# Kernel tuning notes

Hardware: AMD Instinct MI355X
Metric: run time of the kernel (lower is better)

The kernel has to match this reference:

```python
import jax, jax.numpy as jnp
import numpy as np

B = 32       # batch
IN_N = 32    # input capsules
IN_D = 16    # input capsule dim (== out_d)
H = 14       # input spatial
OUT_N = 32   # output capsules
OUT_D = 16
HO = 7       # parent grid h_out = w_out
HID = 64     # Linformer projection dim
EPS = 1e-5


def _gconv(x, w, groups):
    # x: [b, C, H, W], w: [C_out, C_in/groups, kh, kw]; stride 1, pad 1
    return jax.lax.conv_general_dilated(
        x, w, window_strides=(1, 1), padding=((1, 1), (1, 1)),
        dimension_numbers=("NCHW", "OIHW", "NCHW"), feature_group_count=groups)


def setup_inputs() -> dict:
    key = jax.random.key(0)
    ks = jax.random.split(key, 7)
    current_pose = jax.random.normal(ks[0], (B, IN_N, H, H, IN_D), dtype=jnp.float32)
    next_pose = jax.random.normal(ks[1], (B, OUT_N, HO, HO, OUT_D), dtype=jnp.float32)
    # grouped conv weights (torch layout OIHW, groups = IN_N)
    current_w = 0.05 * jax.random.normal(ks[2], (IN_N * IN_D, IN_D, 3, 3), dtype=jnp.float32)
    next_w = 0.05 * jax.random.normal(ks[3], (OUT_N * OUT_D, OUT_N * OUT_D // IN_N, 3, 3), dtype=jnp.float32)
    E_proj = 0.02 * jax.random.normal(ks[4], (IN_N, H * H, HID), dtype=jnp.float32)
    rel_embedd = jax.random.normal(ks[5], (IN_D, HO * HO), dtype=jnp.float32)
    ln_gamma = jnp.ones((OUT_D,), dtype=jnp.float32)
    ln_beta = jnp.zeros((OUT_D,), dtype=jnp.float32)
    return {
        "current_pose": current_pose, "next_pose": next_pose,
        "current_w": current_w, "next_w": next_w,
        "E_proj": E_proj, "rel_embedd": rel_embedd,
        "ln_gamma": ln_gamma, "ln_beta": ln_beta,
        "num_iter": 1,
    }


def reference(current_pose, next_pose, current_w, next_w, E_proj, rel_embedd,
              ln_gamma, ln_beta, num_iter):
    b = current_pose.shape[0]
    # 5D -> [b, n*d, H, W]
    cp = current_pose.transpose(0, 2, 3, 1, 4).reshape(b, H, H, IN_N * IN_D)
    cp = cp.transpose(0, 3, 1, 2)
    cp = _gconv(cp, current_w, IN_N)                       # [b, n*d, H, H]
    # headwise Linformer key projection
    cp = cp.reshape(b, IN_D, IN_N, 1, H * H)
    k = jnp.matmul(cp, E_proj)                             # [b, d, n, 1, HID]
    k = k.reshape(b, IN_D, IN_N * HID).transpose(0, 2, 1)  # [b, n*HID, d]
    rel = jnp.broadcast_to(rel_embedd.T[None], (b, HO * HO, IN_D))
    k = jnp.concatenate([k, rel], axis=1)                  # [b, N, d]

    # parent pose -> queries
    q = next_pose.transpose(0, 2, 3, 1, 4).reshape(b, HO, HO, OUT_N * OUT_D)
    q = q.transpose(0, 3, 1, 2)
    q = _gconv(q, next_w, IN_N)                            # [b, out_n*out_d, HO, HO]
    q = q.reshape(b, OUT_N * HO * HO, OUT_D)               # [b, J, d]

    dots = jnp.einsum("bje,bie->bji", q, k) * (IN_D ** -0.5)  # [b, J, N]
    dots = jax.nn.softmax(dots, axis=-2)                   # softmax over queries j
    out = jnp.einsum("bji,bie->bje", dots, k)              # [b, J, d]

    out = out.reshape(b, OUT_N * IN_D, HO, HO)
    out = _gconv(out, next_w, IN_N)
    out = out.reshape(b, OUT_N, HO, HO, IN_D)

    # LayerNorm over last dim (dropout rate = 0)
    mu = out.mean(-1, keepdims=True)
    var = ((out - mu) ** 2).mean(-1, keepdims=True)
    out = (out - mu) / jnp.sqrt(var + EPS) * ln_gamma + ln_beta
    return out
```

## Files before the change

kernel.cpp:

```cpp
#include <hip/hip_runtime.h>

typedef unsigned short u16;
typedef __attribute__((ext_vector_type(8))) short short8;
typedef __attribute__((ext_vector_type(4))) float floatx4;

#define MFMA16(a, b, c) __builtin_amdgcn_mfma_f32_16x16x32_bf16(a, b, c, 0, 0, 0)

__device__ inline u16 bf16rn(float x) {
    unsigned u = __float_as_uint(x);
    u += 0x7fffu + ((u >> 16) & 1u);
    return (u16)(u >> 16);
}
__device__ inline float bf16tof(u16 h) { return __uint_as_float(((unsigned)h) << 16); }
__device__ inline short8 ld8(const u16* p) { return *(const short8*)p; }

__global__ __launch_bounds__(256) void k_conv14(const float* __restrict__ pose,
                                                const float* __restrict__ w,
                                                float* __restrict__ out) {
    int blk = blockIdx.x;
    int tid = threadIdx.x;
    __shared__ float patch[16 * 256];
#pragma unroll
    for (int k = 0; k < 16; ++k) patch[k * 256 + tid] = 0.f;
    __syncthreads();
    const float* pin = pose + (size_t)blk * 3136;
    for (int t = tid; t < 3136; t += 256) {
        int p = t >> 4, ic = t & 15;
        int y = p / 14, x = p % 14;
        patch[ic * 256 + (y + 1) * 16 + (x + 1)] = pin[t];
    }
    __syncthreads();
    int g = blk & 31;
    const float* wg = w + (size_t)g * 2304;
    float* po = out + (size_t)blk * 3136;
    if (tid < 196) {
        int y = tid / 14, x = tid % 14;
        int base = (y + 1) * 16 + (x + 1);
        float acc[16];
#pragma unroll
        for (int oc = 0; oc < 16; ++oc) acc[oc] = 0.f;
        for (int ic = 0; ic < 16; ++ic) {
            const float* pr = patch + ic * 256 + base;
            float win[9];
#pragma unroll
            for (int ky = 0; ky < 3; ++ky)
#pragma unroll
                for (int kx = 0; kx < 3; ++kx)
                    win[ky * 3 + kx] = pr[(ky - 1) * 16 + (kx - 1)];
            const float* wi = wg + ic * 9;
#pragma unroll
            for (int oc = 0; oc < 16; ++oc)
#pragma unroll
                for (int kk = 0; kk < 9; ++kk)
                    acc[oc] += win[kk] * wi[oc * 144 + kk];
        }
#pragma unroll
        for (int oc = 0; oc < 16; ++oc) po[oc * 196 + tid] = acc[oc];
    }
}

__global__ __launch_bounds__(64) void k_conv7(const float* __restrict__ in,
                                              const float* __restrict__ in2,
                                              const float* __restrict__ w,
                                              float* __restrict__ out, int mode) {
    int blk = blockIdx.x;
    int oh = blk & 1, bg = blk >> 1;
    int tid = threadIdx.x;
    __shared__ float patch[16 * 144];
    for (int t = tid; t < 16 * 144; t += 64) patch[t] = 0.f;
    __syncthreads();
    const float* pin = in + (size_t)bg * 784;
    if (mode == 1) {
        for (int t = tid; t < 784; t += 64) {
            int p = t >> 4, ic = t & 15;
            int y = p / 7, x = p % 7;
            patch[ic * 144 + (y + 1) * 16 + (x + 1)] = pin[t];
        }
    } else {
        const float* pin2 = in2 + (size_t)bg * 784;
        for (int t = tid; t < 784; t += 64) {
            int ic = t / 49, p = t % 49;
            int y = p / 7, x = p % 7;
            patch[ic * 144 + (y + 1) * 16 + (x + 1)] = pin[t] + pin2[t];
        }
    }
    __syncthreads();
    int g = bg & 31;
    const float* wg = w + (size_t)g * 2304 + (size_t)oh * 8 * 144;
    float* po = out + (size_t)bg * 784 + (size_t)oh * 8 * 49;
    if (tid < 49) {
        int y = tid / 7, x = tid % 7;
        int base = (y + 1) * 16 + (x + 1);
        float acc[8];
#pragma unroll
        for (int oc = 0; oc < 8; ++oc) acc[oc] = 0.f;
        for (int ic = 0; ic < 16; ++ic) {
            const float* pr = patch + ic * 144 + base;
            float win[9];
#pragma unroll
            for (int ky = 0; ky < 3; ++ky)
#pragma unroll
                for (int kx = 0; kx < 3; ++kx)
                    win[ky * 3 + kx] = pr[(ky - 1) * 16 + (kx - 1)];
            const float* wi = wg + ic * 9;
#pragma unroll
            for (int oc = 0; oc < 8; ++oc)
#pragma unroll
                for (int kk = 0; kk < 9; ++kk)
                    acc[oc] += win[kk] * wi[oc * 144 + kk];
        }
#pragma unroll
        for (int oc = 0; oc < 8; ++oc) po[oc * 49 + tid] = acc[oc];
    }
}

__global__ __launch_bounds__(256) void k_ecvt(const float* __restrict__ E,
                                              u16* __restrict__ EhT,
                                              u16* __restrict__ ElT) {
    __shared__ float ep[196 * 65];
    int m = blockIdx.x, tid = threadIdx.x;
    const float* eb = E + (size_t)m * 12544;
    for (int t = tid; t < 12544; t += 256) {
        int p = t >> 6, h = t & 63;
        ep[p * 65 + h] = eb[t];
    }
    __syncthreads();
    for (int t = tid; t < 64 * 224; t += 256) {
        int h = t / 224, p = t % 224;
        float v = (p < 196) ? ep[p * 65 + h] : 0.f;
        u16 hi = bf16rn(v);
        u16 lo = bf16rn(v - bf16tof(hi));
        EhT[(size_t)m * 14336 + t] = hi;
        ElT[(size_t)m * 14336 + t] = lo;
    }
}

__global__ __launch_bounds__(256) void k_kproj2(const float* __restrict__ cpconv,
                                                const u16* __restrict__ EhT,
                                                const u16* __restrict__ ElT,
                                                u16* __restrict__ Kh,
                                                u16* __restrict__ Kl,
                                                u16* __restrict__ KhT,
                                                u16* __restrict__ KlT) {
    int blk = blockIdx.x;
    int b = blk >> 5, m = blk & 31;
    int wave = threadIdx.x >> 6, lane = threadIdx.x & 63;
    int ht = wave;
    int n = lane & 15, quad = lane >> 4;

    const float* arow = cpconv + ((size_t)b * 512 + (size_t)n * 32 + m) * 196;
    const u16* bhrow = EhT + ((size_t)m * 64 + ht * 16 + n) * 224;
    const u16* blrow = ElT + ((size_t)m * 64 + ht * 16 + n) * 224;

    floatx4 c = {0.f, 0.f, 0.f, 0.f};
#pragma unroll
    for (int pc = 0; pc < 7; ++pc) {
        int p0 = pc * 32 + quad * 8;
        float av[8];
        if (p0 <= 188) {
            float4 x = *(const float4*)(arow + p0);
            float4 y = *(const float4*)(arow + p0 + 4);
            av[0]=x.x; av[1]=x.y; av[2]=x.z; av[3]=x.w;
            av[4]=y.x; av[5]=y.y; av[6]=y.z; av[7]=y.w;
        } else {
#pragma unroll
            for (int k2 = 0; k2 < 8; ++k2) av[k2] = (p0 + k2 < 196) ? arow[p0 + k2] : 0.f;
        }
        short8 ah, al;
#pragma unroll
        for (int k2 = 0; k2 < 8; ++k2) {
            u16 h = bf16rn(av[k2]);
            ah[k2] = (short)h;
            al[k2] = (short)bf16rn(av[k2] - bf16tof(h));
        }
        short8 bh = ld8(bhrow + pc * 32 + quad * 8);
        short8 bl = ld8(blrow + pc * 32 + quad * 8);
        c = MFMA16(ah, bh, c);
        c = MFMA16(ah, bl, c);
        c = MFMA16(al, bh, c);
    }
    int i = m * 64 + ht * 16 + n;
    size_t bK = (size_t)b * 2112;
    size_t bT = (size_t)b * 33792;
    u16 h[4], l[4];
#pragma unroll
    for (int r = 0; r < 4; ++r) {
        h[r] = bf16rn(c[r]);
        l[r] = bf16rn(c[r] - bf16tof(h[r]));
    }
    *(uint2*)(Kh + (bK + i) * 16 + quad * 4) =
        make_uint2((unsigned)h[0] | ((unsigned)h[1] << 16), (unsigned)h[2] | ((unsigned)h[3] << 16));
    *(uint2*)(Kl + (bK + i) * 16 + quad * 4) =
        make_uint2((unsigned)l[0] | ((unsigned)l[1] << 16), (unsigned)l[2] | ((unsigned)l[3] << 16));
#pragma unroll
    for (int r = 0; r < 4; ++r) {
        KhT[bT + (size_t)(quad * 4 + r) * 2112 + i] = h[r];
        KlT[bT + (size_t)(quad * 4 + r) * 2112 + i] = l[r];
    }
}

__global__ __launch_bounds__(256) void k_cvt(const float* __restrict__ qconv,
                                             const float* __restrict__ rel,
                                             u16* __restrict__ Qp,
                                             u16* __restrict__ Kh,
                                             u16* __restrict__ Kl,
                                             u16* __restrict__ KhT,
                                             u16* __restrict__ KlT) {
    int blk = blockIdx.x, tid = threadIdx.x;
    if (blk < 196) {
        int gid = blk * 256 + tid;
        const float4* q4 = (const float4*)(qconv + (size_t)gid * 16);
        float4 t0 = q4[0], t1 = q4[1], t2 = q4[2], t3 = q4[3];
        float v[16] = {t0.x,t0.y,t0.z,t0.w, t1.x,t1.y,t1.z,t1.w,
                       t2.x,t2.y,t2.z,t2.w, t3.x,t3.y,t3.z,t3.w};
        unsigned hw[8], lw[8];
#pragma unroll
        for (int t = 0; t < 8; ++t) {
            float x0 = v[2*t] * 0.25f, x1 = v[2*t+1] * 0.25f;
            u16 h0 = bf16rn(x0), h1 = bf16rn(x1);
            u16 l0 = bf16rn(x0 - bf16tof(h0)), l1 = bf16rn(x1 - bf16tof(h1));
            hw[t] = (unsigned)h0 | ((unsigned)h1 << 16);
            lw[t] = (unsigned)l0 | ((unsigned)l1 << 16);
        }
        uint4* r4 = (uint4*)(Qp + (size_t)gid * 32);
        r4[0] = make_uint4(hw[0], hw[1], hw[2], hw[3]);
        r4[1] = make_uint4(hw[4], hw[5], hw[6], hw[7]);
        r4[2] = make_uint4(lw[0], lw[1], lw[2], lw[3]);
        r4[3] = make_uint4(lw[4], lw[5], lw[6], lw[7]);
    } else {
        int b = blk - 196;
        size_t bK = (size_t)b * 2112;
        size_t bT = (size_t)b * 33792;
#pragma unroll
        for (int k = 0; k < 4; ++k) {
            int idx = tid + k * 256;
            int row = idx >> 4, e = idx & 15;
            int i = 2048 + row;
            float v = (row < 49) ? rel[e * 49 + row] : 0.f;
            u16 h = bf16rn(v);
            u16 l = bf16rn(v - bf16tof(h));
            Kh[(bK + i) * 16 + e] = h;
            Kl[(bK + i) * 16 + e] = l;
            KhT[bT + (size_t)e * 2112 + i] = h;
            KlT[bT + (size_t)e * 2112 + i] = l;
        }
    }
}

__global__ __launch_bounds__(256) void k_stats4(const u16* __restrict__ Qp,
                                                const u16* __restrict__ Kh,
                                                const u16* __restrict__ Kl,
                                                float* __restrict__ dpart) {
    int blk = blockIdx.x;
    int b = blk / 34; int rem = blk % 34; int jh = rem / 17; int tb = rem % 17;
    int wave = threadIdx.x >> 6, lane = threadIdx.x & 63;
    int it2 = tb * 4 + wave;
    if (it2 >= 66) return;
    int ibase = it2 * 32;
    int n = lane & 15, quad = lane >> 4;
    size_t bK = (size_t)b * 2112;
    const u16* kb = Kh + (bK + ibase + n) * 16 + (quad & 1) * 8;
    const u16* lb = Kl + (bK + ibase + n) * 16 + (quad & 1) * 8;
    short8 bh0 = ld8(kb), bh1 = ld8(kb + 256);
    short8 bl0 = ld8(lb), bl1 = ld8(lb + 256);
    const u16* qb = Qp + (size_t)b * 50176 + (size_t)jh * 49 * 512 + n * 32 + quad * 8;
    floatx4 d0 = {0.f,0.f,0.f,0.f}, d1 = {0.f,0.f,0.f,0.f};
    short8 a0 = ld8(qb), a1 = ld8(qb + 512);
    for (int c = 0; c < 49; ++c) {
        short8 a2 = (c + 2 < 49) ? ld8(qb + (size_t)(c + 2) * 512) : a0;
        floatx4 s0 = {0.f,0.f,0.f,0.f}, s1 = {0.f,0.f,0.f,0.f};
        s0 = MFMA16(a0, bh0, s0);
        s0 = MFMA16(a0, bl0, s0);
        s1 = MFMA16(a0, bh1, s1);
        s1 = MFMA16(a0, bl1, s1);
        d0.x += __expf(s0.x); d0.y += __expf(s0.y);
        d0.z += __expf(s0.z); d0.w += __expf(s0.w);
        d1.x += __expf(s1.x); d1.y += __expf(s1.y);
        d1.z += __expf(s1.z); d1.w += __expf(s1.w);
        a0 = a1; a1 = a2;
    }
    float t0 = d0.x + d0.y + d0.z + d0.w;
    float t1 = d1.x + d1.y + d1.z + d1.w;
    t0 += __shfl_xor(t0, 16); t0 += __shfl_xor(t0, 32);
    t1 += __shfl_xor(t1, 16); t1 += __shfl_xor(t1, 32);
    if (quad == 0) {
        dpart[(size_t)jh * 67584 + bK + ibase + n]      = t0;
        dpart[(size_t)jh * 67584 + bK + ibase + 16 + n] = t1;
    }
}

__global__ __launch_bounds__(256) void k_pv4(const u16* __restrict__ Qp,
                                             const u16* __restrict__ Kh,
                                             const u16* __restrict__ Kl,
                                             const u16* __restrict__ KhT,
                                             const u16* __restrict__ KlT,
                                             const float* __restrict__ dpart,
                                             float* __restrict__ opart) {
    __shared__ __align__(16) u16 sH[2][32][2][8];
    __shared__ __align__(16) u16 sL[2][32][2][8];
    __shared__ __align__(16) u16 tH[2][16][32];
    __shared__ __align__(16) u16 tL[2][16][32];
    __shared__ __align__(16) unsigned wbuf[4][16][36];
    __shared__ float rll[2][32];

    int blk = blockIdx.x;
    int b = blk / 50; int rem = blk % 50; int jtb = rem >> 1; int ih = rem & 1;
    int tid = threadIdx.x, wave = tid >> 6, lane = tid & 63;
    int n = lane & 15, quad = lane >> 4, qh = quad & 1;
    int jt = jtb * 4 + wave;
    int jtc = jt < 98 ? jt : 97;
    int i0 = ih * 1056;
    size_t bK = (size_t)b * 2112;
    size_t bT = (size_t)b * 33792;
    const float* d0p = dpart + bK;
    const float* d1p = dpart + 67584 + bK;

    short8 aq = ld8(Qp + ((size_t)b * 1568 + (size_t)jtc * 16 + n) * 32 + quad * 8);

    int role = wave, L = lane;
    uint4 sreg; float dv = 1.f;
    auto ldchunk = [&](int c) {
        int i0c = i0 + c * 32;
        if (role == 0)      sreg = *(const uint4*)(Kh  + (bK + i0c + (L >> 1)) * 16 + (L & 1) * 8);
        else if (role == 1) sreg = *(const uint4*)(Kl  + (bK + i0c + (L >> 1)) * 16 + (L & 1) * 8);
        else if (role == 2) sreg = *(const uint4*)(KhT + bT + (size_t)(L >> 2) * 2112 + i0c + (L & 3) * 8);
        else {
            sreg = *(const uint4*)(KlT + bT + (size_t)(L >> 2) * 2112 + i0c + (L & 3) * 8);
            if (L < 32) dv = d0p[i0c + L] + d1p[i0c + L];
        }
    };
    auto stchunk = [&](int bf) {
        if (role == 0)      *(uint4*)(&sH[bf][L >> 1][L & 1][0]) = sreg;
        else if (role == 1) *(uint4*)(&sL[bf][L >> 1][L & 1][0]) = sreg;
        else if (role == 2) *(uint4*)(&tH[bf][L >> 2][(L & 3) * 8]) = sreg;
        else {
            *(uint4*)(&tL[bf][L >> 2][(L & 3) * 8]) = sreg;
            if (L < 32) rll[bf][L] = 1.0f / dv;
        }
    };

    floatx4 o = {0.f, 0.f, 0.f, 0.f};

    ldchunk(0); stchunk(0); ldchunk(1);
    __syncthreads();
    for (int c = 0; c < 33; ++c) {
        int cb = c & 1;
        short8 sh0 = ld8(&sH[cb][n][qh][0]);
        short8 sh1 = ld8(&sH[cb][16 + n][qh][0]);
        short8 sl0 = ld8(&sL[cb][n][qh][0]);
        short8 sl1 = ld8(&sL[cb][16 + n][qh][0]);
        short8 th  = ld8(&tH[cb][n][quad * 8]);
        short8 tl  = ld8(&tL[cb][n][quad * 8]);
        float r0 = rll[cb][n], r1 = rll[cb][16 + n];
        floatx4 s0 = {0.f,0.f,0.f,0.f};
        s0 = MFMA16(aq, sh0, s0);
        s0 = MFMA16(aq, sl0, s0);
        floatx4 s1 = {0.f,0.f,0.f,0.f};
        s1 = MFMA16(aq, sh1, s1);
        s1 = MFMA16(aq, sl1, s1);
#pragma unroll
        for (int r = 0; r < 4; ++r) {
            float w0 = __expf(s0[r]) * r0;
            float w1 = __expf(s1[r]) * r1;
            unsigned u0 = __float_as_uint(w0), u1 = __float_as_uint(w1);
            unsigned h0 = u0 & 0xffff0000u, h1 = u1 & 0xffff0000u;
            float l0 = w0 - __uint_as_float(h0);
            float l1 = w1 - __uint_as_float(h1);
            wbuf[wave][quad * 4 + r][n]      = h0 | (__float_as_uint(l0) >> 16);
            wbuf[wave][quad * 4 + r][16 + n] = h1 | (__float_as_uint(l1) >> 16);
        }
        asm volatile("s_waitcnt lgkmcnt(0)" ::: "memory");
        uint4 wa = *(const uint4*)(&wbuf[wave][n][quad * 8]);
        uint4 wb = *(const uint4*)(&wbuf[wave][n][quad * 8 + 4]);
        union { unsigned u[4]; short8 s; } hv, lv;
        hv.u[0] = (wa.x >> 16) | (wa.y & 0xffff0000u);
        hv.u[1] = (wa.z >> 16) | (wa.w & 0xffff0000u);
        hv.u[2] = (wb.x >> 16) | (wb.y & 0xffff0000u);
        hv.u[3] = (wb.z >> 16) | (wb.w & 0xffff0000u);
        lv.u[0] = (wa.x & 0xffffu) | (wa.y << 16);
        lv.u[1] = (wa.z & 0xffffu) | (wa.w << 16);
        lv.u[2] = (wb.x & 0xffffu) | (wb.y << 16);
        lv.u[3] = (wb.z & 0xffffu) | (wb.w << 16);
        o = MFMA16(hv.s, th, o);
        o = MFMA16(hv.s, tl, o);
        o = MFMA16(lv.s, th, o);
        if (c < 32) stchunk((c + 1) & 1);
        if (c < 31) ldchunk(c + 2);
        __syncthreads();
    }
    if (jt < 98) {
        float* ob = opart + (size_t)ih * 802816 + ((size_t)b * 1568 + (size_t)jt * 16) * 16;
#pragma unroll
        for (int r = 0; r < 4; ++r) ob[(quad * 4 + r) * 16 + n] = o[r];
    }
}

__global__ __launch_bounds__(256) void k_ln(const float* __restrict__ x,
                                            const float* __restrict__ gamma,
                                            const float* __restrict__ beta,
                                            float* __restrict__ out, int ngroups) {
    int g = blockIdx.x * 256 + threadIdx.x;
    if (g >= ngroups) return;
    const float4* xp = (const float4*)(x + (size_t)g * 16);
    float4 x0 = xp[0], x1 = xp[1], x2 = xp[2], x3 = xp[3];
    float sum = x0.x + x0.y + x0.z + x0.w + x1.x + x1.y + x1.z + x1.w
              + x2.x + x2.y + x2.z + x2.w + x3.x + x3.y + x3.z + x3.w;
    float mu = sum * 0.0625f;
    float var = 0.f;
    var += (x0.x-mu)*(x0.x-mu) + (x0.y-mu)*(x0.y-mu) + (x0.z-mu)*(x0.z-mu) + (x0.w-mu)*(x0.w-mu);
    var += (x1.x-mu)*(x1.x-mu) + (x1.y-mu)*(x1.y-mu) + (x1.z-mu)*(x1.z-mu) + (x1.w-mu)*(x1.w-mu);
    var += (x2.x-mu)*(x2.x-mu) + (x2.y-mu)*(x2.y-mu) + (x2.z-mu)*(x2.z-mu) + (x2.w-mu)*(x2.w-mu);
    var += (x3.x-mu)*(x3.x-mu) + (x3.y-mu)*(x3.y-mu) + (x3.z-mu)*(x3.z-mu) + (x3.w-mu)*(x3.w-mu);
    float rstd = rsqrtf(var * 0.0625f + 1e-5f);
    const float4* gp = (const float4*)gamma;
    const float4* bp = (const float4*)beta;
    float4 g0 = gp[0], g1 = gp[1], g2 = gp[2], g3 = gp[3];
    float4 be0 = bp[0], be1 = bp[1], be2 = bp[2], be3 = bp[3];
    float4 o0, o1, o2, o3;
    o0.x = (x0.x-mu)*rstd*g0.x + be0.x; o0.y = (x0.y-mu)*rstd*g0.y + be0.y;
    o0.z = (x0.z-mu)*rstd*g0.z + be0.z; o0.w = (x0.w-mu)*rstd*g0.w + be0.w;
    o1.x = (x1.x-mu)*rstd*g1.x + be1.x; o1.y = (x1.y-mu)*rstd*g1.y + be1.y;
    o1.z = (x1.z-mu)*rstd*g1.z + be1.z; o1.w = (x1.w-mu)*rstd*g1.w + be1.w;
    o2.x = (x2.x-mu)*rstd*g2.x + be2.x; o2.y = (x2.y-mu)*rstd*g2.y + be2.y;
    o2.z = (x2.z-mu)*rstd*g2.z + be2.z; o2.w = (x2.w-mu)*rstd*g2.w + be2.w;
    o3.x = (x3.x-mu)*rstd*g3.x + be3.x; o3.y = (x3.y-mu)*rstd*g3.y + be3.y;
    o3.z = (x3.z-mu)*rstd*g3.z + be3.z; o3.w = (x3.w-mu)*rstd*g3.w + be3.w;
    float4* op = (float4*)(out + (size_t)g * 16);
    op[0] = o0; op[1] = o1; op[2] = o2; op[3] = o3;
}

extern "C" void kernel_launch(void* const* d_in, const int* in_sizes, int n_in,
                              void* d_out, int out_size, void* d_ws, size_t ws_size,
                              hipStream_t stream) {
    const float* current_pose = (const float*)d_in[0];
    const float* next_pose    = (const float*)d_in[1];
    const float* current_w    = (const float*)d_in[2];
    const float* next_w       = (const float*)d_in[3];
    const float* E_proj       = (const float*)d_in[4];
    const float* rel          = (const float*)d_in[5];
    const float* ln_gamma     = (const float*)d_in[6];
    const float* ln_beta      = (const float*)d_in[7];
    float* out = (float*)d_out;
    float* ws  = (float*)d_ws;

    float* cpconv = ws;
    float* conv2  = ws;
    float* opart  = ws + 802816;
    float* dpart  = ws + 2408448;
    float* qconv  = ws + 3211264;
    u16*   ub     = (u16*)(ws + 4014080);
    u16* Qp  = ub;
    u16* Kh  = ub + 1605632;
    u16* Kl  = ub + 2686976;
    u16* KhT = ub + 3768320;
    u16* KlT = ub + 4849664;
    u16* EhT = ub + 5931008;
    u16* ElT = ub + 6389760;

    k_conv14<<<1024, 256, 0, stream>>>(current_pose, current_w, cpconv);
    k_conv7 <<<2048, 64,  0, stream>>>(next_pose, next_pose, next_w, qconv, 1);
    k_ecvt  <<<32,   256, 0, stream>>>(E_proj, EhT, ElT);
    k_cvt   <<<228,  256, 0, stream>>>(qconv, rel, Qp, Kh, Kl, KhT, KlT);
    k_kproj2<<<1024, 256, 0, stream>>>(cpconv, EhT, ElT, Kh, Kl, KhT, KlT);
    k_stats4<<<1088, 256, 0, stream>>>(Qp, Kh, Kl, dpart);
    k_pv4   <<<1600, 256, 0, stream>>>(Qp, Kh, Kl, KhT, KlT, dpart, opart);
    k_conv7 <<<2048, 64,  0, stream>>>(opart, opart + 802816, next_w, conv2, 0);
    k_ln    <<<196,  256, 0, stream>>>(conv2, ln_gamma, ln_beta, out, 50176);
}
```

Baseline: 245.0 us.

## Merge preprocessing kernels, split conv14 across output halves, single-bf16 softmax weights

Folds the E_proj conversion, the rel-embedding K rows and a weight re-layout for the 14x14 grouped conv into one preprocessing kernel. conv14 now runs twice as many blocks, each computing 8 output channels with the reordered weights so each block reads a contiguous run of weights. In the PV kernel the softmax weights are truncated to a single bf16 instead of a hi/lo pair, cutting one MFMA and the packing work per chunk. The truncation lowers the accuracy of the attention output, and halving conv14 means each input patch is loaded twice.

```diff
diff --git a/kernel.cpp b/kernel.cpp
--- a/kernel.cpp
+++ b/kernel.cpp
@@ -14,31 +14,88 @@
 __device__ inline float bf16tof(u16 h) { return __uint_as_float(((unsigned)h) << 16); }
 __device__ inline short8 ld8(const u16* p) { return *(const short8*)p; }
 
+__global__ __launch_bounds__(256) void k_ecvt2(const float* __restrict__ E,
+                                               const float* __restrict__ rel,
+                                               const float* __restrict__ w,
+                                               u16* __restrict__ EhT,
+                                               u16* __restrict__ ElT,
+                                               u16* __restrict__ Kh,
+                                               u16* __restrict__ Kl,
+                                               u16* __restrict__ KhT,
+                                               u16* __restrict__ KlT,
+                                               float* __restrict__ w2) {
+    int blk = blockIdx.x, tid = threadIdx.x;
+    if (blk < 32) {
+        __shared__ float ep[196 * 65];
+        int m = blk;
+        const float* eb = E + (size_t)m * 12544;
+        for (int t = tid; t < 12544; t += 256) {
+            int p = t >> 6, h = t & 63;
+            ep[p * 65 + h] = eb[t];
+        }
+        __syncthreads();
+        for (int t = tid; t < 64 * 224; t += 256) {
+            int h = t / 224, p = t % 224;
+            float v = (p < 196) ? ep[p * 65 + h] : 0.f;
+            u16 hi = bf16rn(v);
+            u16 lo = bf16rn(v - bf16tof(hi));
+            EhT[(size_t)m * 14336 + t] = hi;
+            ElT[(size_t)m * 14336 + t] = lo;
+        }
+    } else if (blk < 64) {
+        int b = blk - 32;
+        size_t bK = (size_t)b * 2112;
+        size_t bT = (size_t)b * 33792;
+#pragma unroll
+        for (int k = 0; k < 4; ++k) {
+            int idx = tid + k * 256;
+            int row = idx >> 4, e = idx & 15;
+            int i = 2048 + row;
+            float v = (row < 49) ? rel[e * 49 + row] : 0.f;
+            u16 h = bf16rn(v);
+            u16 l = bf16rn(v - bf16tof(h));
+            Kh[(bK + i) * 16 + e] = h;
+            Kl[(bK + i) * 16 + e] = l;
+            KhT[bT + (size_t)e * 2112 + i] = h;
+            KlT[bT + (size_t)e * 2112 + i] = l;
+        }
+    } else {
+        int g0 = (blk - 64) * 4;
+        for (int t = tid; t < 4 * 2304; t += 256) {
+            int g = g0 + t / 2304, r = t % 2304;
+            int oc = r / 144, rr = r % 144;
+            w2[(size_t)g * 2304 + (rr / 9) * 144 + oc * 9 + (rr % 9)] =
+                w[(size_t)g * 2304 + r];
+        }
+    }
+}
+
 __global__ __launch_bounds__(256) void k_conv14(const float* __restrict__ pose,
-                                                const float* __restrict__ w,
+                                                const float* __restrict__ w2,
                                                 float* __restrict__ out) {
     int blk = blockIdx.x;
+    int oh = blk & 1, bg = blk >> 1;
     int tid = threadIdx.x;
     __shared__ float patch[16 * 256];
 #pragma unroll
     for (int k = 0; k < 16; ++k) patch[k * 256 + tid] = 0.f;
     __syncthreads();
-    const float* pin = pose + (size_t)blk * 3136;
+    const float* pin = pose + (size_t)bg * 3136;
     for (int t = tid; t < 3136; t += 256) {
         int p = t >> 4, ic = t & 15;
         int y = p / 14, x = p % 14;
         patch[ic * 256 + (y + 1) * 16 + (x + 1)] = pin[t];
     }
     __syncthreads();
-    int g = blk & 31;
-    const float* wg = w + (size_t)g * 2304;
-    float* po = out + (size_t)blk * 3136;
+    int g = bg & 31;
+    const float* wg = w2 + (size_t)g * 2304 + oh * 72;
+    float* po = out + (size_t)bg * 3136 + oh * 8 * 196;
     if (tid < 196) {
         int y = tid / 14, x = tid % 14;
         int base = (y + 1) * 16 + (x + 1);
-        float acc[16];
-#pragma unroll
-        for (int oc = 0; oc < 16; ++oc) acc[oc] = 0.f;
+        float acc[8];
+#pragma unroll
+        for (int oc = 0; oc < 8; ++oc) acc[oc] = 0.f;
         for (int ic = 0; ic < 16; ++ic) {
             const float* pr = patch + ic * 256 + base;
             float win[9];
@@ -47,15 +104,15 @@
 #pragma unroll
                 for (int kx = 0; kx < 3; ++kx)
                     win[ky * 3 + kx] = pr[(ky - 1) * 16 + (kx - 1)];
-            const float* wi = wg + ic * 9;
-#pragma unroll
-            for (int oc = 0; oc < 16; ++oc)
+            const float* wi = wg + ic * 144;
+#pragma unroll
+            for (int oc = 0; oc < 8; ++oc)
 #pragma unroll
                 for (int kk = 0; kk < 9; ++kk)
-                    acc[oc] += win[kk] * wi[oc * 144 + kk];
-        }
-#pragma unroll
-        for (int oc = 0; oc < 16; ++oc) po[oc * 196 + tid] = acc[oc];
+                    acc[oc] += win[kk] * wi[oc * 9 + kk];
+        }
+#pragma unroll
+        for (int oc = 0; oc < 8; ++oc) po[oc * 196 + tid] = acc[oc];
     }
 }
 
@@ -114,27 +171,6 @@
     }
 }
 
-__global__ __launch_bounds__(256) void k_ecvt(const float* __restrict__ E,
-                                              u16* __restrict__ EhT,
-                                              u16* __restrict__ ElT) {
-    __shared__ float ep[196 * 65];
-    int m = blockIdx.x, tid = threadIdx.x;
-    const float* eb = E + (size_t)m * 12544;
-    for (int t = tid; t < 12544; t += 256) {
-        int p = t >> 6, h = t & 63;
-        ep[p * 65 + h] = eb[t];
-    }
-    __syncthreads();
-    for (int t = tid; t < 64 * 224; t += 256) {
-        int h = t / 224, p = t % 224;
-        float v = (p < 196) ? ep[p * 65 + h] : 0.f;
-        u16 hi = bf16rn(v);
-        u16 lo = bf16rn(v - bf16tof(hi));
-        EhT[(size_t)m * 14336 + t] = hi;
-        ElT[(size_t)m * 14336 + t] = lo;
-    }
-}
-
 __global__ __launch_bounds__(256) void k_kproj2(const float* __restrict__ cpconv,
                                                 const u16* __restrict__ EhT,
                                                 const u16* __restrict__ ElT,
@@ -200,51 +236,26 @@
 }
 
 __global__ __launch_bounds__(256) void k_cvt(const float* __restrict__ qconv,
-                                             const float* __restrict__ rel,
-                                             u16* __restrict__ Qp,
-                                             u16* __restrict__ Kh,
-                                             u16* __restrict__ Kl,
-                                             u16* __restrict__ KhT,
-                                             u16* __restrict__ KlT) {
-    int blk = blockIdx.x, tid = threadIdx.x;
-    if (blk < 196) {
-        int gid = blk * 256 + tid;
-        const float4* q4 = (const float4*)(qconv + (size_t)gid * 16);
-        float4 t0 = q4[0], t1 = q4[1], t2 = q4[2], t3 = q4[3];
-        float v[16] = {t0.x,t0.y,t0.z,t0.w, t1.x,t1.y,t1.z,t1.w,
-                       t2.x,t2.y,t2.z,t2.w, t3.x,t3.y,t3.z,t3.w};
-        unsigned hw[8], lw[8];
-#pragma unroll
-        for (int t = 0; t < 8; ++t) {
-            float x0 = v[2*t] * 0.25f, x1 = v[2*t+1] * 0.25f;
-            u16 h0 = bf16rn(x0), h1 = bf16rn(x1);
-            u16 l0 = bf16rn(x0 - bf16tof(h0)), l1 = bf16rn(x1 - bf16tof(h1));
-            hw[t] = (unsigned)h0 | ((unsigned)h1 << 16);
-            lw[t] = (unsigned)l0 | ((unsigned)l1 << 16);
-        }
-        uint4* r4 = (uint4*)(Qp + (size_t)gid * 32);
-        r4[0] = make_uint4(hw[0], hw[1], hw[2], hw[3]);
-        r4[1] = make_uint4(hw[4], hw[5], hw[6], hw[7]);
-        r4[2] = make_uint4(lw[0], lw[1], lw[2], lw[3]);
-        r4[3] = make_uint4(lw[4], lw[5], lw[6], lw[7]);
-    } else {
-        int b = blk - 196;
-        size_t bK = (size_t)b * 2112;
-        size_t bT = (size_t)b * 33792;
-#pragma unroll
-        for (int k = 0; k < 4; ++k) {
-            int idx = tid + k * 256;
-            int row = idx >> 4, e = idx & 15;
-            int i = 2048 + row;
-            float v = (row < 49) ? rel[e * 49 + row] : 0.f;
-            u16 h = bf16rn(v);
-            u16 l = bf16rn(v - bf16tof(h));
-            Kh[(bK + i) * 16 + e] = h;
-            Kl[(bK + i) * 16 + e] = l;
-            KhT[bT + (size_t)e * 2112 + i] = h;
-            KlT[bT + (size_t)e * 2112 + i] = l;
-        }
-    }
+                                             u16* __restrict__ Qp) {
+    int gid = blockIdx.x * 256 + threadIdx.x;
+    const float4* q4 = (const float4*)(qconv + (size_t)gid * 16);
+    float4 t0 = q4[0], t1 = q4[1], t2 = q4[2], t3 = q4[3];
+    float v[16] = {t0.x,t0.y,t0.z,t0.w, t1.x,t1.y,t1.z,t1.w,
+                   t2.x,t2.y,t2.z,t2.w, t3.x,t3.y,t3.z,t3.w};
+    unsigned hw[8], lw[8];
+#pragma unroll
+    for (int t = 0; t < 8; ++t) {
+        float x0 = v[2*t] * 0.25f, x1 = v[2*t+1] * 0.25f;
+        u16 h0 = bf16rn(x0), h1 = bf16rn(x1);
+        u16 l0 = bf16rn(x0 - bf16tof(h0)), l1 = bf16rn(x1 - bf16tof(h1));
+        hw[t] = (unsigned)h0 | ((unsigned)h1 << 16);
+        lw[t] = (unsigned)l0 | ((unsigned)l1 << 16);
+    }
+    uint4* r4 = (uint4*)(Qp + (size_t)gid * 32);
+    r4[0] = make_uint4(hw[0], hw[1], hw[2], hw[3]);
+    r4[1] = make_uint4(hw[4], hw[5], hw[6], hw[7]);
+    r4[2] = make_uint4(lw[0], lw[1], lw[2], lw[3]);
+    r4[3] = make_uint4(lw[4], lw[5], lw[6], lw[7]);
 }
 
 __global__ __launch_bounds__(256) void k_stats4(const u16* __restrict__ Qp,
@@ -289,18 +300,18 @@
     }
 }
 
-__global__ __launch_bounds__(256) void k_pv4(const u16* __restrict__ Qp,
+__global__ __launch_bounds__(256) void k_pv5(const u16* __restrict__ Qp,
                                              const u16* __restrict__ Kh,
                                              const u16* __restrict__ Kl,
                                              const u16* __restrict__ KhT,
                                              const u16* __restrict__ KlT,
                                              const float* __restrict__ dpart,
                                              float* __restrict__ opart) {
-    __shared__ __align__(16) u16 sH[2][32][2][8];
-    __shared__ __align__(16) u16 sL[2][32][2][8];
+    __shared__ __align__(16) u16 sH[2][32][16];
+    __shared__ __align__(16) u16 sL[2][32][16];
     __shared__ __align__(16) u16 tH[2][16][32];
     __shared__ __align__(16) u16 tL[2][16][32];
-    __shared__ __align__(16) unsigned wbuf[4][16][36];
+    __shared__ __align__(16) u16 w16[4][16][40];
     __shared__ float rll[2][32];
 
     int blk = blockIdx.x;
@@ -330,8 +341,8 @@
         }
     };
     auto stchunk = [&](int bf) {
-        if (role == 0)      *(uint4*)(&sH[bf][L >> 1][L & 1][0]) = sreg;
-        else if (role == 1) *(uint4*)(&sL[bf][L >> 1][L & 1][0]) = sreg;
+        if (role == 0)      *(uint4*)(&sH[bf][L >> 1][(L & 1) * 8]) = sreg;
+        else if (role == 1) *(uint4*)(&sL[bf][L >> 1][(L & 1) * 8]) = sreg;
         else if (role == 2) *(uint4*)(&tH[bf][L >> 2][(L & 3) * 8]) = sreg;
         else {
             *(uint4*)(&tL[bf][L >> 2][(L & 3) * 8]) = sreg;
@@ -345,10 +356,10 @@
     __syncthreads();
     for (int c = 0; c < 33; ++c) {
         int cb = c & 1;
-        short8 sh0 = ld8(&sH[cb][n][qh][0]);
-        short8 sh1 = ld8(&sH[cb][16 + n][qh][0]);
-        short8 sl0 = ld8(&sL[cb][n][qh][0]);
-        short8 sl1 = ld8(&sL[cb][16 + n][qh][0]);
+        short8 sh0 = ld8(&sH[cb][n][qh * 8]);
+        short8 sh1 = ld8(&sH[cb][16 + n][qh * 8]);
+        short8 sl0 = ld8(&sL[cb][n][qh * 8]);
+        short8 sl1 = ld8(&sL[cb][16 + n][qh * 8]);
         short8 th  = ld8(&tH[cb][n][quad * 8]);
         short8 tl  = ld8(&tL[cb][n][quad * 8]);
         float r0 = rll[cb][n], r1 = rll[cb][16 + n];
@@ -362,28 +373,13 @@
         for (int r = 0; r < 4; ++r) {
             float w0 = __expf(s0[r]) * r0;
             float w1 = __expf(s1[r]) * r1;
-            unsigned u0 = __float_as_uint(w0), u1 = __float_as_uint(w1);
-            unsigned h0 = u0 & 0xffff0000u, h1 = u1 & 0xffff0000u;
-            float l0 = w0 - __uint_as_float(h0);
-            float l1 = w1 - __uint_as_float(h1);
-            wbuf[wave][quad * 4 + r][n]      = h0 | (__float_as_uint(l0) >> 16);
-            wbuf[wave][quad * 4 + r][16 + n] = h1 | (__float_as_uint(l1) >> 16);
+            w16[wave][quad * 4 + r][n]      = (u16)(__float_as_uint(w0) >> 16);
+            w16[wave][quad * 4 + r][16 + n] = (u16)(__float_as_uint(w1) >> 16);
         }
         asm volatile("s_waitcnt lgkmcnt(0)" ::: "memory");
-        uint4 wa = *(const uint4*)(&wbuf[wave][n][quad * 8]);
-        uint4 wb = *(const uint4*)(&wbuf[wave][n][quad * 8 + 4]);
-        union { unsigned u[4]; short8 s; } hv, lv;
-        hv.u[0] = (wa.x >> 16) | (wa.y & 0xffff0000u);
-        hv.u[1] = (wa.z >> 16) | (wa.w & 0xffff0000u);
-        hv.u[2] = (wb.x >> 16) | (wb.y & 0xffff0000u);
-        hv.u[3] = (wb.z >> 16) | (wb.w & 0xffff0000u);
-        lv.u[0] = (wa.x & 0xffffu) | (wa.y << 16);
-        lv.u[1] = (wa.z & 0xffffu) | (wa.w << 16);
-        lv.u[2] = (wb.x & 0xffffu) | (wb.y << 16);
-        lv.u[3] = (wb.z & 0xffffu) | (wb.w << 16);
-        o = MFMA16(hv.s, th, o);
-        o = MFMA16(hv.s, tl, o);
-        o = MFMA16(lv.s, th, o);
+        short8 aw = ld8(&w16[wave][n][quad * 8]);
+        o = MFMA16(aw, th, o);
+        o = MFMA16(aw, tl, o);
         if (c < 32) stchunk((c + 1) & 1);
         if (c < 31) ldchunk(c + 2);
         __syncthreads();
@@ -448,7 +444,8 @@
     float* opart  = ws + 802816;
     float* dpart  = ws + 2408448;
     float* qconv  = ws + 3211264;
-    u16*   ub     = (u16*)(ws + 4014080);
+    float* w2     = ws + 4014080;
+    u16*   ub     = (u16*)(ws + 4087808);
     u16* Qp  = ub;
     u16* Kh  = ub + 1605632;
     u16* Kl  = ub + 2686976;
@@ -457,13 +454,14 @@
     u16* EhT = ub + 5931008;
     u16* ElT = ub + 6389760;
 
-    k_conv14<<<1024, 256, 0, stream>>>(current_pose, current_w, cpconv);
+    k_ecvt2 <<<72,   256, 0, stream>>>(E_proj, rel, current_w, EhT, ElT,
+                                       Kh, Kl, KhT, KlT, w2);
+    k_conv14<<<2048, 256, 0, stream>>>(current_pose, w2, cpconv);
     k_conv7 <<<2048, 64,  0, stream>>>(next_pose, next_pose, next_w, qconv, 1);
-    k_ecvt  <<<32,   256, 0, stream>>>(E_proj, EhT, ElT);
-    k_cvt   <<<228,  256, 0, stream>>>(qconv, rel, Qp, Kh, Kl, KhT, KlT);
+    k_cvt   <<<196,  256, 0, stream>>>(qconv, Qp);
     k_kproj2<<<1024, 256, 0, stream>>>(cpconv, EhT, ElT, Kh, Kl, KhT, KlT);
     k_stats4<<<1088, 256, 0, stream>>>(Qp, Kh, Kl, dpart);
-    k_pv4   <<<1600, 256, 0, stream>>>(Qp, Kh, Kl, KhT, KlT, dpart, opart);
+    k_pv5   <<<1600, 256, 0, stream>>>(Qp, Kh, Kl, KhT, KlT, dpart, opart);
     k_conv7 <<<2048, 64,  0, stream>>>(opart, opart + 802816, next_w, conv2, 0);
     k_ln    <<<196,  256, 0, stream>>>(conv2, ln_gamma, ln_beta, out, 50176);
 }
```

New measurement: 232.3 us. 1.05x faster.
